# Kernel tuning notes

Hardware: AMD Instinct MI355X
Metric: run time of the kernel (lower is better)

## Reference

```python
import jax, jax.numpy as jnp
import numpy as np
from math import comb

LEVEL = 16
LENGTH = 64
TOPK = 2
SIZE = 512
BATCH = 32
NEG = -1e8


def _catalan(n_leaves):
    # number of distinct binary trees over n_leaves leaves
    m = n_leaves - 1
    return comb(2 * m, m) // (m + 1)


def _offsets(length, level):
    # cell offset of each chart level: level l occupies (length - l) cells
    return np.cumsum([0] + [length - l for l in range(level)])


def setup_inputs() -> dict:
    key = jax.random.key(0)
    K, B, size, level, length = TOPK, BATCH, SIZE, LEVEL, LENGTH
    L, N = length - level, level
    off = _offsets(length, level)
    ncells = int(off[-1])
    ks = jax.random.split(key, 5)
    chart_h = jax.random.normal(ks[0], (K, B, ncells, size), jnp.float32)
    chart_s = jax.random.normal(ks[1], (K, B, ncells, 1), jnp.float32)
    mat = jax.random.normal(ks[2], (size, size), jnp.float32) / np.sqrt(size).astype(np.float32)
    Wc = jax.random.normal(ks[3], (2 * size, size), jnp.float32) / np.sqrt(2 * size).astype(np.float32)
    bc = jnp.zeros((size,), jnp.float32)
    # structural gather indices: left child = (level n, pos), right child = (level level-1-n, pos+n+1)
    l_idx = np.zeros((L, N), np.int64)
    r_idx = np.zeros((L, N), np.int64)
    for pos in range(L):
        for n in range(N):
            l_idx[pos, n] = off[n] + pos
            r_idx[pos, n] = off[level - 1 - n] + pos + n + 1
    return {
        'chart_h': chart_h, 'chart_s': chart_s,
        'l_index': jnp.asarray(l_idx.reshape(-1)), 'r_index': jnp.asarray(r_idx.reshape(-1)),
        'mat': mat, 'Wc': Wc, 'bc': bc,
    }


def _penalty_mask(level, N, K):
    # Faithful to penalize_incomplete_splits: idx = i // K**2 == 0 for i < K*K,
    # so only the n_idx==0 block is ever penalized. l_level=0, r_level=level-1.
    M = N * K * K
    mask = np.zeros(M, bool)
    for i in range(K * K):
        lk, rk = i // K, i % K
        if _catalan(0 + 1) < lk + 1 or _catalan((level - 1) + 1) < rk + 1:
            mask[i] = True
    return jnp.asarray(mask)


def reference(chart_h, chart_s, l_index, r_index, mat, Wc, bc):
    K, B, ncells, size = chart_h.shape
    level = LEVEL
    N = level
    L = l_index.shape[0] // N
    M = N * K * K
    # gather child states from charts: (K,B,L,N,size) -> (B,L,N,K,size)
    lh = jnp.moveaxis(chart_h[:, :, l_index].reshape(K, B, L, N, size), 0, 3)
    rh = jnp.moveaxis(chart_h[:, :, r_index].reshape(K, B, L, N, size), 0, 3)
    ls = jnp.moveaxis(chart_s[:, :, l_index].reshape(K, B, L, N), 0, 3)  # (B,L,N,K)
    rs = jnp.moveaxis(chart_s[:, :, r_index].reshape(K, B, L, N), 0, 3)
    # bilinear composition score: (B,L,N,K_l,K_r)
    s_raw = jnp.einsum('blnkd,de,blnje->blnkj', lh, mat, rh)
    # flat combo index = n*K*K + lk*K + rk; add child scores
    s = (s_raw + ls[..., :, None] + rs[..., None, :]).reshape(B, L, M)
    s = jnp.where(_penalty_mask(level, N, K), jnp.float32(NEG), s)
    topk_s, topk_idx = jax.lax.top_k(s, K)  # (B,L,K), sorted descending like torch.topk
    # dense compose over all N*K*K combos
    combo_lh = jnp.repeat(lh, K, axis=3).reshape(B, L, M, size)   # lk = z // K
    combo_rh = jnp.tile(rh, (1, 1, 1, K, 1)).reshape(B, L, M, size)  # rk = z % K
    all_h = jnp.tanh(jnp.concatenate([combo_lh, combo_rh], axis=-1) @ Wc + bc)
    topk_h = jnp.take_along_axis(all_h, topk_idx[..., None], axis=2)  # (B,L,K,size)
    # UnitNorm normalize_func
    topk_h = topk_h / jnp.linalg.norm(topk_h, axis=-1, keepdims=True)
    topk_s = topk_s[..., None]  # (B,L,K,1) to match torch shape
    if _catalan(N + 1) < K:  # static no-op at this level
        topk_s = topk_s.at[:, :, _catalan(N + 1):].set(NEG)
    topk_n_idx = topk_idx // (K * K)
    topk_lk = (topk_idx % (K * K)) // K
    topk_rk = (topk_idx % (K * K)) % K
    return topk_h, topk_s, topk_n_idx, topk_lk, topk_rk
```

## Files before the change

### kernel.cpp

```cpp
#include <hip/hip_runtime.h>
#include <cstdint>
#include <cstddef>

#define B_DIM   32
#define L_DIM   48
#define NCELLS  904
#define SZ      512
#define NEGF    (-1e8f)
#define DELTA   0.25f
#define MAXC    32

#define OFF_S   1572864
#define OFF_N   1575936
#define OFF_L   1579008
#define OFF_R   1582080

typedef _Float16  f16x8 __attribute__((ext_vector_type(8)));
typedef float     f32x4 __attribute__((ext_vector_type(4)));

static __device__ __forceinline__ uint16_t f2bf(float f) {
    uint32_t u = __builtin_bit_cast(uint32_t, f);
    u += 0x7fffu + ((u >> 16) & 1u);
    return (uint16_t)(u >> 16);
}

#define GLD16(gp, lp) __builtin_amdgcn_global_load_lds(                        \
        (__attribute__((address_space(1))) void*)(gp),                         \
        (__attribute__((address_space(3))) void*)(lp), 16, 0, 0)

static __device__ __forceinline__ int level_off(int n) {
    return n * 64 - (n * (n - 1)) / 2;
}

__global__ __launch_bounds__(256)
void prep_mat(const float* __restrict__ mat, _Float16* __restrict__ P)
{
    const int tg   = blockIdx.x * 256 + threadIdx.x;
    const int c    = tg >> 6, lane = tg & 63;
    const int srow = 16 * (c & 31) + (lane & 15);
    const int scol = 32 * (c >> 5) + (lane >> 4) * 8;
    const float4 a = *(const float4*)(mat + (size_t)srow * 512 + scol);
    const float4 b = *(const float4*)(mat + (size_t)srow * 512 + scol + 4);
    f16x8 w;
    w[0]=(_Float16)(a.x*64.f); w[1]=(_Float16)(a.y*64.f);
    w[2]=(_Float16)(a.z*64.f); w[3]=(_Float16)(a.w*64.f);
    w[4]=(_Float16)(b.x*64.f); w[5]=(_Float16)(b.y*64.f);
    w[6]=(_Float16)(b.z*64.f); w[7]=(_Float16)(b.w*64.f);
    *(f16x8*)(P + (size_t)tg * 8) = w;
}

__global__ __launch_bounds__(256, 3)
void gemm_fused(const float* __restrict__ A,
                const _Float16* __restrict__ P,
                _Float16* __restrict__ C)
{
    __shared__ _Float16 As16[8 * 512];
    __shared__ _Float16 Bs[32 * 512];

    const int t = threadIdx.x;
    const int wave = t >> 6, lane = t & 63;
    const int n0 = blockIdx.x * 256;
    const int nq = n0 >> 4;
    const int m0 = blockIdx.y * 64;
    const int col_l = lane & 15, quad = lane >> 4;
    const int stag = blockIdx.y & 7;

    f32x4 acc[4][4];
#pragma unroll
    for (int i = 0; i < 4; ++i)
#pragma unroll
        for (int j = 0; j < 4; ++j) acc[i][j] = (f32x4){0.f, 0.f, 0.f, 0.f};

    for (int ks = 0; ks < 8; ++ks) {
        const int kse = (ks + stag) & 7;
        __syncthreads();

        f32x4 p0[2], p1[2];
#pragma unroll
        for (int h = 0; h < 2; ++h) {
            const int c  = wave * 2 + h;
            const int kki = c >> 2, mi = c & 3;
            const float* ap = A + (size_t)(m0 + mi * 16 + col_l) * 512
                                + kse * 64 + kki * 32 + quad * 8;
            p0[h] = *(const f32x4*)ap;
            p1[h] = *(const f32x4*)(ap + 4);
        }
#pragma unroll
        for (int i2 = 0; i2 < 8; ++i2) {
            const int idx = wave * 8 + i2;
            const int kki = idx >> 4, i = idx & 15;
            const int c = (kse * 2 + kki) * 32 + nq + i;
            GLD16(P + (size_t)c * 512 + lane * 8, (char*)Bs + idx * 1024);
        }
#pragma unroll
        for (int h = 0; h < 2; ++h) {
            f16x8 av;
#pragma unroll
            for (int j = 0; j < 4; ++j) {
                av[j]     = (_Float16)(p0[h][j] * 16.f);
                av[j + 4] = (_Float16)(p1[h][j] * 16.f);
            }
            *(f16x8*)&As16[(wave * 2 + h) * 512 + lane * 8] = av;
        }
        __syncthreads();

#pragma unroll
        for (int kki = 0; kki < 2; ++kki) {
            f16x8 af[4];
#pragma unroll
            for (int mi = 0; mi < 4; ++mi)
                af[mi] = *(const f16x8*)&As16[(kki * 4 + mi) * 512 + lane * 8];
#pragma unroll
            for (int ni = 0; ni < 4; ++ni) {
                const f16x8 bf = *(const f16x8*)&Bs[(kki * 16 + wave * 4 + ni) * 512 + lane * 8];
#pragma unroll
                for (int mi = 0; mi < 4; ++mi)
                    acc[mi][ni] = __builtin_amdgcn_mfma_f32_16x16x32_f16(
                        af[mi], bf, acc[mi][ni], 0, 0, 0);
            }
        }
    }

#pragma unroll
    for (int ni = 0; ni < 4; ++ni) {
        const int ncol = n0 + wave * 64 + ni * 16 + col_l;
#pragma unroll
        for (int mi = 0; mi < 4; ++mi) {
            const int mrow = m0 + mi * 16 + quad * 4;
#pragma unroll
            for (int r = 0; r < 4; ++r)
                C[(size_t)(mrow + r) * 512 + ncol] = (_Float16)acc[mi][ni][r];
        }
    }
}

static __device__ __forceinline__ void emit_outputs(
    int row, int i1, int i2, float v1, float v2, float* out)
{
    out[OFF_S + row * 2 + 0] = v1;
    out[OFF_S + row * 2 + 1] = v2;
    out[OFF_N + row * 2 + 0] = (float)(i1 >> 2);
    out[OFF_N + row * 2 + 1] = (float)(i2 >> 2);
    out[OFF_L + row * 2 + 0] = (float)((i1 >> 1) & 1);
    out[OFF_L + row * 2 + 1] = (float)((i2 >> 1) & 1);
    out[OFF_R + row * 2 + 0] = (float)(i1 & 1);
    out[OFF_R + row * 2 + 1] = (float)(i2 & 1);
}

static __device__ __forceinline__ void gather_x(
    int row, int pos, int b, const int* top_z,
    const float* __restrict__ chart_h, uint16_t* __restrict__ X, int tid)
{
#pragma unroll
    for (int kq = 0; kq < 2; ++kq) {
        const int z = top_z[kq];
        const int n = z >> 2, lk = (z >> 1) & 1, rk = z & 1;
        const int lcell = level_off(n) + pos;
        const int rcell = level_off(15 - n) + pos + n + 1;
        const float* srcl = chart_h + ((size_t)(lk * B_DIM + b) * NCELLS + lcell) * SZ;
        const float* srcr = chart_h + ((size_t)(rk * B_DIM + b) * NCELLS + rcell) * SZ;
        uint16_t* dst = X + ((size_t)row * 2 + kq) * 1024;
        const int e = tid * 2;
        const float2 a = *(const float2*)(srcl + e);
        const float2 c = *(const float2*)(srcr + e);
        *(uint32_t*)(dst + e)       = (uint32_t)f2bf(a.x) | ((uint32_t)f2bf(a.y) << 16);
        *(uint32_t*)(dst + 512 + e) = (uint32_t)f2bf(c.x) | ((uint32_t)f2bf(c.y) << 16);
    }
}

__global__ __launch_bounds__(256)
void score_topk(const float* __restrict__ chart_h,
                const _Float16* __restrict__ T16,
                const float* __restrict__ chart_s,
                uint32_t* __restrict__ items,
                int* __restrict__ rowbase,
                int* __restrict__ counter,
                int* __restrict__ flags,
                uint16_t* __restrict__ X,
                float* __restrict__ out)
{
    const int b   = blockIdx.x / L_DIM;
    const int pos = blockIdx.x % L_DIM;
    const int row = blockIdx.x;
    const int wave = threadIdx.x >> 6, lane = threadIdx.x & 63;

    __shared__ float s_sh[64];
    __shared__ int top_z[2];
    __shared__ int flag_sh;

#pragma unroll
    for (int ni = 0; ni < 4; ++ni) {
        const int n = wave * 4 + ni;
        const int lcell = level_off(n) + pos;
        const int rcell = level_off(15 - n) + pos + n + 1;

        const float* lp0 = chart_h + ((size_t)(0 * B_DIM + b) * NCELLS + lcell) * SZ + lane * 8;
        const float* lp1 = chart_h + ((size_t)(1 * B_DIM + b) * NCELLS + lcell) * SZ + lane * 8;
        const float4 l0a = *(const float4*)lp0, l0b = *(const float4*)(lp0 + 4);
        const float4 l1a = *(const float4*)lp1, l1b = *(const float4*)(lp1 + 4);
        const f16x8 t0 = *(const f16x8*)(T16 + ((size_t)(0 * B_DIM + b) * NCELLS + rcell) * SZ + lane * 8);
        const f16x8 t1 = *(const f16x8*)(T16 + ((size_t)(1 * B_DIM + b) * NCELLS + rcell) * SZ + lane * 8);

        float l0[8] = {l0a.x, l0a.y, l0a.z, l0a.w, l0b.x, l0b.y, l0b.z, l0b.w};
        float l1[8] = {l1a.x, l1a.y, l1a.z, l1a.w, l1b.x, l1b.y, l1b.z, l1b.w};

        float d00 = 0.f, d01 = 0.f, d10 = 0.f, d11 = 0.f;
#pragma unroll
        for (int j = 0; j < 8; ++j) {
            const float c0 = (float)t0[j], c1 = (float)t1[j];
            d00 += l0[j] * c0; d01 += l0[j] * c1;
            d10 += l1[j] * c0; d11 += l1[j] * c1;
        }
#pragma unroll
        for (int o = 32; o > 0; o >>= 1) {
            d00 += __shfl_down(d00, o);
            d01 += __shfl_down(d01, o);
            d10 += __shfl_down(d10, o);
            d11 += __shfl_down(d11, o);
        }
        if (lane == 0) {
            const float ls0 = chart_s[(size_t)(0 * B_DIM + b) * NCELLS + lcell];
            const float ls1 = chart_s[(size_t)(1 * B_DIM + b) * NCELLS + lcell];
            const float rs0 = chart_s[(size_t)(0 * B_DIM + b) * NCELLS + rcell];
            const float rs1 = chart_s[(size_t)(1 * B_DIM + b) * NCELLS + rcell];
            const float inv = 1.0f / 1024.0f;
            s_sh[n * 4 + 0] = d00 * inv + ls0 + rs0;
            s_sh[n * 4 + 1] = d01 * inv + ls0 + rs1;
            s_sh[n * 4 + 2] = d10 * inv + ls1 + rs0;
            s_sh[n * 4 + 3] = d11 * inv + ls1 + rs1;
        }
    }
    __syncthreads();

    if (threadIdx.x < 64) {
        float v = s_sh[lane];
        if (lane == 2 || lane == 3) v = NEGF;
        float v1 = v; int i1 = lane;
#pragma unroll
        for (int o = 32; o > 0; o >>= 1) {
            float ov = __shfl_down(v1, o);
            int   oi = __shfl_down(i1, o);
            if (ov > v1 || (ov == v1 && oi < i1)) { v1 = ov; i1 = oi; }
        }
        v1 = __shfl(v1, 0); i1 = __shfl(i1, 0);
        float v2 = (lane == i1) ? -3.4e38f : v; int i2 = lane;
#pragma unroll
        for (int o = 32; o > 0; o >>= 1) {
            float ov = __shfl_down(v2, o);
            int   oi = __shfl_down(i2, o);
            if (ov > v2 || (ov == v2 && oi < i2)) { v2 = ov; i2 = oi; }
        }
        v2 = __shfl(v2, 0); i2 = __shfl(i2, 0);
        float v3 = (lane == i1 || lane == i2) ? -3.4e38f : v;
#pragma unroll
        for (int o = 32; o > 0; o >>= 1) {
            const float ov = __shfl_down(v3, o);
            if (ov > v3) v3 = ov;
        }
        v3 = __shfl(v3, 0);

        const int f = (v1 - v2 < DELTA) || (v2 - v3 < DELTA);
        const bool cand = (v >= v2 - DELTA);
        const unsigned long long mask = __ballot(cand);
        const int nc_full = __popcll(mask);
        const int nc = nc_full < MAXC ? nc_full : MAXC;
        int base = 0;
        if (lane == 0) {
            flags[row] = f ? nc : 0;
            flag_sh = f;
            if (f) base = atomicAdd(counter, nc);
            rowbase[row] = base;
            top_z[0] = i1; top_z[1] = i2;
            if (!f) emit_outputs(row, i1, i2, v1, v2, out);
        }
        base = __shfl(base, 0);
        if (f && cand) {
            const int rank = __popcll(mask & ((1ull << lane) - 1ull));
            if (rank < MAXC) items[base + rank] = ((uint32_t)row << 6) | (uint32_t)lane;
        }
    }
    __syncthreads();

    if (!flag_sh)
        gather_x(row, pos, b, top_z, chart_h, X, threadIdx.x);
}

__global__ __launch_bounds__(256)
void refine_eval(const float* __restrict__ chart_h,
                 const float* __restrict__ chart_s,
                 const float* __restrict__ mat,
                 const uint32_t* __restrict__ items,
                 const int* __restrict__ counter,
                 float* __restrict__ exval)
{
    const int total = *counter;
    const int t = threadIdx.x;
    const int wave = t >> 6, lane = t & 63;

    __shared__ float lh_sh[2][512];
    __shared__ float psum[2][4];

    for (int p = blockIdx.x; 2 * p < total; p += gridDim.x) {
        const int it0 = 2 * p;
        const int it1v = (2 * p + 1 < total);
        const uint32_t item0 = items[it0];
        const uint32_t item1 = it1v ? items[it0 + 1] : item0;

        int rowA = item0 >> 6, zA = item0 & 63;
        int bA = rowA / L_DIM, posA = rowA % L_DIM;
        int nA = zA >> 2, lkA = (zA >> 1) & 1, rkA = zA & 1;
        int lcA = level_off(nA) + posA, rcA = level_off(15 - nA) + posA + nA + 1;
        int rowB = item1 >> 6, zB = item1 & 63;
        int bB = rowB / L_DIM, posB = rowB % L_DIM;
        int nB = zB >> 2, lkB = (zB >> 1) & 1, rkB = zB & 1;
        int lcB = level_off(nB) + posB, rcB = level_off(15 - nB) + posB + nB + 1;

        const float* lhA = chart_h + ((size_t)(lkA * B_DIM + bA) * NCELLS + lcA) * SZ;
        const float* rhA = chart_h + ((size_t)(rkA * B_DIM + bA) * NCELLS + rcA) * SZ;
        const float* lhB = chart_h + ((size_t)(lkB * B_DIM + bB) * NCELLS + lcB) * SZ;
        const float* rhB = chart_h + ((size_t)(rkB * B_DIM + bB) * NCELLS + rcB) * SZ;

        __syncthreads();
        lh_sh[0][t] = lhA[t]; lh_sh[0][t + 256] = lhA[t + 256];
        lh_sh[1][t] = lhB[t]; lh_sh[1][t + 256] = lhB[t + 256];
        const float4 rA0 = *(const float4*)(rhA + lane * 8);
        const float4 rA1 = *(const float4*)(rhA + lane * 8 + 4);
        const float4 rB0 = *(const float4*)(rhB + lane * 8);
        const float4 rB1 = *(const float4*)(rhB + lane * 8 + 4);
        __syncthreads();

        const float* mb = mat + (size_t)(wave * 128) * 512 + lane * 8;
        float a00 = 0.f, a01 = 0.f, b00 = 0.f, b01 = 0.f;
        for (int e = 0; e < 128; e += 2) {
            const float4 m0 = *(const float4*)(mb + (size_t)(e + 0) * 512);
            const float4 m1 = *(const float4*)(mb + (size_t)(e + 0) * 512 + 4);
            const float4 m2 = *(const float4*)(mb + (size_t)(e + 1) * 512);
            const float4 m3 = *(const float4*)(mb + (size_t)(e + 1) * 512 + 4);
            const int eg = wave * 128 + e;
            const float lA0 = lh_sh[0][eg],     lB0 = lh_sh[1][eg];
            const float lA1 = lh_sh[0][eg + 1], lB1 = lh_sh[1][eg + 1];
            const float dA0 = m0.x*rA0.x + m0.y*rA0.y + m0.z*rA0.z + m0.w*rA0.w
                            + m1.x*rA1.x + m1.y*rA1.y + m1.z*rA1.z + m1.w*rA1.w;
            const float dB0 = m0.x*rB0.x + m0.y*rB0.y + m0.z*rB0.z + m0.w*rB0.w
                            + m1.x*rB1.x + m1.y*rB1.y + m1.z*rB1.z + m1.w*rB1.w;
            const float dA1 = m2.x*rA0.x + m2.y*rA0.y + m2.z*rA0.z + m2.w*rA0.w
                            + m3.x*rA1.x + m3.y*rA1.y + m3.z*rA1.z + m3.w*rA1.w;
            const float dB1 = m2.x*rB0.x + m2.y*rB0.y + m2.z*rB0.z + m2.w*rB0.w
                            + m3.x*rB1.x + m3.y*rB1.y + m3.z*rB1.z + m3.w*rB1.w;
            a00 += lA0 * dA0; a01 += lA1 * dA1;
            b00 += lB0 * dB0; b01 += lB1 * dB1;
        }
        float sA = a00 + a01, sB = b00 + b01;
#pragma unroll
        for (int o = 32; o > 0; o >>= 1) {
            sA += __shfl_down(sA, o);
            sB += __shfl_down(sB, o);
        }
        if (lane == 0) { psum[0][wave] = sA; psum[1][wave] = sB; }
        __syncthreads();
        if (t == 0) {
            const float lsA = chart_s[(size_t)(lkA * B_DIM + bA) * NCELLS + lcA];
            const float rsA = chart_s[(size_t)(rkA * B_DIM + bA) * NCELLS + rcA];
            exval[it0] = psum[0][0] + psum[0][1] + psum[0][2] + psum[0][3] + lsA + rsA;
            if (it1v) {
                const float lsB = chart_s[(size_t)(lkB * B_DIM + bB) * NCELLS + lcB];
                const float rsB = chart_s[(size_t)(rkB * B_DIM + bB) * NCELLS + rcB];
                exval[it0 + 1] = psum[1][0] + psum[1][1] + psum[1][2] + psum[1][3] + lsB + rsB;
            }
        }
    }
}

__global__ __launch_bounds__(256)
void refine_pick(const float* __restrict__ chart_h,
                 const uint32_t* __restrict__ items,
                 const int* __restrict__ rowbase,
                 const int* __restrict__ flags,
                 const float* __restrict__ exval,
                 uint16_t* __restrict__ X,
                 float* __restrict__ out)
{
    const int row = blockIdx.x;
    const int nc = flags[row];
    if (nc == 0) return;
    const int b = row / L_DIM, pos = row % L_DIM;
    const int t = threadIdx.x;

    __shared__ int top_z[2];

    if (t == 0) {
        const int base = rowbase[row];
        float v1 = -3.4e38f; int c1 = -1;
        for (int c = 0; c < nc; ++c) {
            const float v = exval[base + c];
            if (v > v1) { v1 = v; c1 = c; }
        }
        float v2 = -3.4e38f; int c2 = -1;
        for (int c = 0; c < nc; ++c) {
            if (c == c1) continue;
            const float v = exval[base + c];
            if (v > v2) { v2 = v; c2 = c; }
        }
        const int i1 = (int)(items[base + c1] & 63u);
        const int i2 = (int)(items[base + c2] & 63u);
        top_z[0] = i1; top_z[1] = i2;
        emit_outputs(row, i1, i2, v1, v2, out);
    }
    __syncthreads();
    gather_x(row, pos, b, top_z, chart_h, X, t);
}

__global__ __launch_bounds__(256)
void transpose_wc(const float* __restrict__ Wc, uint16_t* __restrict__ WcT)
{
    __shared__ float tbuf[64][65];
    const int i0 = blockIdx.x * 64;
    const int o0 = blockIdx.y * 64;
    const int c = threadIdx.x & 63, r4 = threadIdx.x >> 6;
    for (int rr = r4; rr < 64; rr += 4)
        tbuf[rr][c] = Wc[(size_t)(i0 + rr) * 512 + o0 + c];
    __syncthreads();
    for (int rr = r4; rr < 64; rr += 4)
        WcT[(size_t)(o0 + rr) * 1024 + i0 + c] = f2bf(tbuf[c][rr]);
}

typedef __bf16 bf16x8 __attribute__((ext_vector_type(8)));

__global__ __launch_bounds__(256, 2)
void gemm_compose(const uint16_t* __restrict__ A,
                  const uint16_t* __restrict__ Bm,
                  const float* __restrict__ bias,
                  float* __restrict__ C,
                  int M, int Nn, int Kk)
{
    __shared__ uint16_t As[128 * 64];
    __shared__ uint16_t Bs[128 * 64];

    const int tid  = threadIdx.x;
    const int wave = tid >> 6, lane = tid & 63;
    const int m0 = blockIdx.x * 128, n0 = blockIdx.y * 128;
    const int wm = (wave & 1) * 64, wn = (wave >> 1) * 64;
    const int col_l = lane & 15, quad = lane >> 4;
    const int lrow = lane >> 3;
    const int lcol = (lane & 7) * 8;

    f32x4 acc[4][4];
#pragma unroll
    for (int i = 0; i < 4; ++i)
#pragma unroll
        for (int j = 0; j < 4; ++j) acc[i][j] = (f32x4){0.f, 0.f, 0.f, 0.f};

    for (int k0 = 0; k0 < Kk; k0 += 64) {
        __syncthreads();
#pragma unroll
        for (int i = 0; i < 4; ++i) {
            const int q = wave * 4 + i;
            const int r = q * 8 + lrow;
            GLD16(A  + (size_t)(m0 + r) * Kk + k0 + lcol, (char*)As + q * 1024);
            GLD16(Bm + (size_t)(n0 + r) * Kk + k0 + lcol, (char*)Bs + q * 1024);
        }
        __syncthreads();
#pragma unroll
        for (int kk = 0; kk < 64; kk += 32) {
            bf16x8 af[4], bfr[4];
#pragma unroll
            for (int mi = 0; mi < 4; ++mi)
                af[mi] = *(const bf16x8*)&As[(wm + mi * 16 + col_l) * 64 + kk + quad * 8];
#pragma unroll
            for (int ni = 0; ni < 4; ++ni)
                bfr[ni] = *(const bf16x8*)&Bs[(wn + ni * 16 + col_l) * 64 + kk + quad * 8];
#pragma unroll
            for (int mi = 0; mi < 4; ++mi)
#pragma unroll
                for (int ni = 0; ni < 4; ++ni)
                    acc[mi][ni] = __builtin_amdgcn_mfma_f32_16x16x32_bf16(
                        af[mi], bfr[ni], acc[mi][ni], 0, 0, 0);
        }
    }

#pragma unroll
    for (int ni = 0; ni < 4; ++ni) {
        const int ncol = n0 + wn + ni * 16 + col_l;
        const float bv = bias[ncol];
#pragma unroll
        for (int mi = 0; mi < 4; ++mi) {
            const int mrow = m0 + wm + mi * 16 + quad * 4;
#pragma unroll
            for (int r = 0; r < 4; ++r)
                C[(size_t)(mrow + r) * Nn + ncol] = tanhf(acc[mi][ni][r] + bv);
        }
    }
}

__global__ __launch_bounds__(256)
void norm_rows(const float* __restrict__ H, float* __restrict__ out)
{
    const int row = blockIdx.x;
    const float* h = H + (size_t)row * SZ;
    const int t = threadIdx.x;
    const int wave = t >> 6, lane = t & 63;
    const float a = h[t], c = h[t + 256];
    float ss = a * a + c * c;
#pragma unroll
    for (int o = 32; o > 0; o >>= 1) ss += __shfl_down(ss, o);
    __shared__ float wsum[4];
    if (lane == 0) wsum[wave] = ss;
    __syncthreads();
    const float inv = rsqrtf(wsum[0] + wsum[1] + wsum[2] + wsum[3]);
    out[(size_t)row * SZ + t]       = a * inv;
    out[(size_t)row * SZ + t + 256] = c * inv;
}

extern "C" void kernel_launch(void* const* d_in, const int* in_sizes, int n_in,
                              void* d_out, int out_size, void* d_ws, size_t ws_size,
                              hipStream_t stream)
{
    const float* chart_h = (const float*)d_in[0];
    const float* chart_s = (const float*)d_in[1];
    const float* mat = (const float*)d_in[4];
    const float* Wc  = (const float*)d_in[5];
    const float* bc  = (const float*)d_in[6];
    float* out = (float*)d_out;

    char* ws = (char*)d_ws;
    _Float16* T16   = (_Float16*)ws;
    _Float16* MAT16 = (_Float16*)(ws + 59244544);
    uint32_t* ITEMS = (uint32_t*)(ws + 59768832);
    float*    EXVAL = (float*)(ws + 59965440);
    int*      RBASE = (int*)(ws + 60162048);
    int*      CNT   = (int*)(ws + 60168192);
    int*      FLAGS = (int*)(ws + 60168448);
    uint16_t* X     = (uint16_t*)(ws + 60174592);
    uint16_t* WcT   = (uint16_t*)ws;
    float*    H     = (float*)(ws + 1048576);

    hipMemsetAsync(CNT, 0, 4, stream);
    prep_mat<<<dim3(128), 256, 0, stream>>>(mat, MAT16);
    gemm_fused<<<dim3(2, 904), 256, 0, stream>>>(chart_h, MAT16, T16);
    score_topk<<<dim3(B_DIM * L_DIM), 256, 0, stream>>>(chart_h, T16, chart_s,
                                                        ITEMS, RBASE, CNT, FLAGS, X, out);
    transpose_wc<<<dim3(16, 8), 256, 0, stream>>>(Wc, WcT);
    refine_eval<<<dim3(1024), 256, 0, stream>>>(chart_h, chart_s, mat, ITEMS, CNT, EXVAL);
    refine_pick<<<dim3(B_DIM * L_DIM), 256, 0, stream>>>(chart_h, ITEMS, RBASE, FLAGS,
                                                         EXVAL, X, out);
    gemm_compose<<<dim3(24, 4), 256, 0, stream>>>(X, WcT, bc, H, 3072, 512, 1024);
    norm_rows<<<dim3(3072), 256, 0, stream>>>(H, out);
}
```

Baseline: 315.4 us.

## Double-buffer A tile in LDS and read B fragments directly from global

The GEMM kernel now double-buffers the converted fp16 A tile in shared memory, prefetching the next k-slice into registers while MFMAs run on the current one. That leaves one barrier per iteration instead of two. The B operand is no longer staged through LDS: each wave loads its prepacked fragments straight from global memory, which cuts LDS use and may raise occupancy. In exchange, B fragments are no longer shared across the block through LDS and their global load latency sits directly in front of the MFMAs.

```diff
diff --git a/kernel.cpp b/kernel.cpp
--- a/kernel.cpp
+++ b/kernel.cpp
@@ -54,8 +54,7 @@
                 const _Float16* __restrict__ P,
                 _Float16* __restrict__ C)
 {
-    __shared__ _Float16 As16[8 * 512];
-    __shared__ _Float16 Bs[32 * 512];
+    __shared__ _Float16 As16[2][8 * 512];
 
     const int t = threadIdx.x;
     const int wave = t >> 6, lane = t & 63;
@@ -71,54 +70,71 @@
 #pragma unroll
         for (int j = 0; j < 4; ++j) acc[i][j] = (f32x4){0.f, 0.f, 0.f, 0.f};
 
+    const int c0 = wave * 2, c1 = wave * 2 + 1;
+    const float* ab0 = A + (size_t)(m0 + (c0 & 3) * 16 + col_l) * 512
+                         + (c0 >> 2) * 32 + quad * 8;
+    const float* ab1 = A + (size_t)(m0 + (c1 & 3) * 16 + col_l) * 512
+                         + (c1 >> 2) * 32 + quad * 8;
+
+    {
+        const int kse = stag;
+        const f32x4 q0a = *(const f32x4*)(ab0 + kse * 64);
+        const f32x4 q0b = *(const f32x4*)(ab0 + kse * 64 + 4);
+        const f32x4 q1a = *(const f32x4*)(ab1 + kse * 64);
+        const f32x4 q1b = *(const f32x4*)(ab1 + kse * 64 + 4);
+        f16x8 av0, av1;
+#pragma unroll
+        for (int j = 0; j < 4; ++j) {
+            av0[j] = (_Float16)(q0a[j] * 16.f); av0[j + 4] = (_Float16)(q0b[j] * 16.f);
+            av1[j] = (_Float16)(q1a[j] * 16.f); av1[j + 4] = (_Float16)(q1b[j] * 16.f);
+        }
+        *(f16x8*)&As16[0][c0 * 512 + lane * 8] = av0;
+        *(f16x8*)&As16[0][c1 * 512 + lane * 8] = av1;
+        __syncthreads();
+    }
+
     for (int ks = 0; ks < 8; ++ks) {
+        const int cur = ks & 1;
         const int kse = (ks + stag) & 7;
-        __syncthreads();
-
-        f32x4 p0[2], p1[2];
-#pragma unroll
-        for (int h = 0; h < 2; ++h) {
-            const int c  = wave * 2 + h;
-            const int kki = c >> 2, mi = c & 3;
-            const float* ap = A + (size_t)(m0 + mi * 16 + col_l) * 512
-                                + kse * 64 + kki * 32 + quad * 8;
-            p0[h] = *(const f32x4*)ap;
-            p1[h] = *(const f32x4*)(ap + 4);
-        }
-#pragma unroll
-        for (int i2 = 0; i2 < 8; ++i2) {
-            const int idx = wave * 8 + i2;
-            const int kki = idx >> 4, i = idx & 15;
-            const int c = (kse * 2 + kki) * 32 + nq + i;
-            GLD16(P + (size_t)c * 512 + lane * 8, (char*)Bs + idx * 1024);
-        }
-#pragma unroll
-        for (int h = 0; h < 2; ++h) {
-            f16x8 av;
-#pragma unroll
-            for (int j = 0; j < 4; ++j) {
-                av[j]     = (_Float16)(p0[h][j] * 16.f);
-                av[j + 4] = (_Float16)(p1[h][j] * 16.f);
-            }
-            *(f16x8*)&As16[(wave * 2 + h) * 512 + lane * 8] = av;
-        }
-        __syncthreads();
+        const bool notlast = (ks < 7);
+
+        f32x4 n0a = {}, n0b = {}, n1a = {}, n1b = {};
+        if (notlast) {
+            const int ksn = (ks + 1 + stag) & 7;
+            n0a = *(const f32x4*)(ab0 + ksn * 64);
+            n0b = *(const f32x4*)(ab0 + ksn * 64 + 4);
+            n1a = *(const f32x4*)(ab1 + ksn * 64);
+            n1b = *(const f32x4*)(ab1 + ksn * 64 + 4);
+        }
 
 #pragma unroll
         for (int kki = 0; kki < 2; ++kki) {
             f16x8 af[4];
 #pragma unroll
             for (int mi = 0; mi < 4; ++mi)
-                af[mi] = *(const f16x8*)&As16[(kki * 4 + mi) * 512 + lane * 8];
+                af[mi] = *(const f16x8*)&As16[cur][(kki * 4 + mi) * 512 + lane * 8];
 #pragma unroll
             for (int ni = 0; ni < 4; ++ni) {
-                const f16x8 bf = *(const f16x8*)&Bs[(kki * 16 + wave * 4 + ni) * 512 + lane * 8];
+                const int c = (kse * 2 + kki) * 32 + nq + wave * 4 + ni;
+                const f16x8 bf = *(const f16x8*)(P + (size_t)c * 512 + lane * 8);
 #pragma unroll
                 for (int mi = 0; mi < 4; ++mi)
                     acc[mi][ni] = __builtin_amdgcn_mfma_f32_16x16x32_f16(
                         af[mi], bf, acc[mi][ni], 0, 0, 0);
             }
         }
+
+        if (notlast) {
+            f16x8 av0, av1;
+#pragma unroll
+            for (int j = 0; j < 4; ++j) {
+                av0[j] = (_Float16)(n0a[j] * 16.f); av0[j + 4] = (_Float16)(n0b[j] * 16.f);
+                av1[j] = (_Float16)(n1a[j] * 16.f); av1[j + 4] = (_Float16)(n1b[j] * 16.f);
+            }
+            *(f16x8*)&As16[cur ^ 1][c0 * 512 + lane * 8] = av0;
+            *(f16x8*)&As16[cur ^ 1][c1 * 512 + lane * 8] = av1;
+        }
+        __syncthreads();
     }
 
 #pragma unroll
```

Result: no change. 321.2 us (+1.8%).

## Stage full A tile in swizzled LDS and stream B fragments from global

Applied to the files above, without the earlier changes.

The GEMM kernel now loads the whole 64x512 A tile into LDS once, converting to fp16 and XOR-swizzling it to avoid bank conflicts, with a single barrier. The per-k-step loop with two barriers and LDS staging of B is removed; each wave reads its pre-packed B fragments directly from global memory (expected to hit in L2/cache). This drops the synchronization in the k loop, but LDS use grows to 64KB, so occupancy is lowered to 2 blocks per CU, and B reads are no longer shared through LDS.

```diff
diff --git a/kernel.cpp b/kernel.cpp
--- a/kernel.cpp
+++ b/kernel.cpp
@@ -49,13 +49,12 @@
     *(f16x8*)(P + (size_t)tg * 8) = w;
 }
 
-__global__ __launch_bounds__(256, 3)
+__global__ __launch_bounds__(256, 2)
 void gemm_fused(const float* __restrict__ A,
                 const _Float16* __restrict__ P,
                 _Float16* __restrict__ C)
 {
-    __shared__ _Float16 As16[8 * 512];
-    __shared__ _Float16 Bs[32 * 512];
+    __shared__ _Float16 As16[64 * 512];
 
     const int t = threadIdx.x;
     const int wave = t >> 6, lane = t & 63;
@@ -63,7 +62,33 @@
     const int nq = n0 >> 4;
     const int m0 = blockIdx.y * 64;
     const int col_l = lane & 15, quad = lane >> 4;
-    const int stag = blockIdx.y & 7;
+
+    {
+        const int r  = lane;
+        const int cw = wave;
+        const float* ap = A + (size_t)(m0 + r) * 512 + cw * 128;
+        _Float16* drow = As16 + r * 512;
+        const int swz = r & 7;
+#pragma unroll 2
+        for (int s = 0; s < 8; ++s) {
+            const f32x4 a0 = *(const f32x4*)(ap + s * 16);
+            const f32x4 a1 = *(const f32x4*)(ap + s * 16 + 4);
+            const f32x4 a2 = *(const f32x4*)(ap + s * 16 + 8);
+            const f32x4 a3 = *(const f32x4*)(ap + s * 16 + 12);
+            f16x8 v0, v1;
+#pragma unroll
+            for (int j = 0; j < 4; ++j) {
+                v0[j]     = (_Float16)(a0[j] * 16.f);
+                v0[j + 4] = (_Float16)(a1[j] * 16.f);
+                v1[j]     = (_Float16)(a2[j] * 16.f);
+                v1[j + 4] = (_Float16)(a3[j] * 16.f);
+            }
+            const int u0 = cw * 16 + s * 2;
+            *(f16x8*)&drow[(u0 ^ swz) * 8]       = v0;
+            *(f16x8*)&drow[((u0 + 1) ^ swz) * 8] = v1;
+        }
+    }
+    __syncthreads();
 
     f32x4 acc[4][4];
 #pragma unroll
@@ -71,53 +96,23 @@
 #pragma unroll
         for (int j = 0; j < 4; ++j) acc[i][j] = (f32x4){0.f, 0.f, 0.f, 0.f};
 
-    for (int ks = 0; ks < 8; ++ks) {
-        const int kse = (ks + stag) & 7;
-        __syncthreads();
-
-        f32x4 p0[2], p1[2];
-#pragma unroll
-        for (int h = 0; h < 2; ++h) {
-            const int c  = wave * 2 + h;
-            const int kki = c >> 2, mi = c & 3;
-            const float* ap = A + (size_t)(m0 + mi * 16 + col_l) * 512
-                                + kse * 64 + kki * 32 + quad * 8;
-            p0[h] = *(const f32x4*)ap;
-            p1[h] = *(const f32x4*)(ap + 4);
-        }
-#pragma unroll
-        for (int i2 = 0; i2 < 8; ++i2) {
-            const int idx = wave * 8 + i2;
-            const int kki = idx >> 4, i = idx & 15;
-            const int c = (kse * 2 + kki) * 32 + nq + i;
-            GLD16(P + (size_t)c * 512 + lane * 8, (char*)Bs + idx * 1024);
-        }
-#pragma unroll
-        for (int h = 0; h < 2; ++h) {
-            f16x8 av;
-#pragma unroll
-            for (int j = 0; j < 4; ++j) {
-                av[j]     = (_Float16)(p0[h][j] * 16.f);
-                av[j + 4] = (_Float16)(p1[h][j] * 16.f);
-            }
-            *(f16x8*)&As16[(wave * 2 + h) * 512 + lane * 8] = av;
-        }
-        __syncthreads();
-
-#pragma unroll
-        for (int kki = 0; kki < 2; ++kki) {
-            f16x8 af[4];
+#pragma unroll 4
+    for (int w16 = 0; w16 < 16; ++w16) {
+        f16x8 af[4];
+#pragma unroll
+        for (int mi = 0; mi < 4; ++mi) {
+            const int r = mi * 16 + col_l;
+            const int u = w16 * 4 + quad;
+            af[mi] = *(const f16x8*)&As16[r * 512 + (u ^ (r & 7)) * 8];
+        }
+#pragma unroll
+        for (int ni = 0; ni < 4; ++ni) {
+            const int c = w16 * 32 + nq + wave * 4 + ni;
+            const f16x8 bf = *(const f16x8*)(P + (size_t)c * 512 + lane * 8);
 #pragma unroll
             for (int mi = 0; mi < 4; ++mi)
-                af[mi] = *(const f16x8*)&As16[(kki * 4 + mi) * 512 + lane * 8];
-#pragma unroll
-            for (int ni = 0; ni < 4; ++ni) {
-                const f16x8 bf = *(const f16x8*)&Bs[(kki * 16 + wave * 4 + ni) * 512 + lane * 8];
-#pragma unroll
-                for (int mi = 0; mi < 4; ++mi)
-                    acc[mi][ni] = __builtin_amdgcn_mfma_f32_16x16x32_f16(
-                        af[mi], bf, acc[mi][ni], 0, 0, 0);
-            }
+                acc[mi][ni] = __builtin_amdgcn_mfma_f32_16x16x32_f16(
+                    af[mi], bf, acc[mi][ni], 0, 0, 0);
         }
     }
 
```

After: 322.2 us. +2.2%, slower.
